# Optimization experiments

Hardware: AMD Instinct MI355X
Metric: run time of the kernel (lower is better)

Reference implementation:

```python
import jax, jax.numpy as jnp
import numpy as np

QMAX = 32767.0   # 2**15 - 1
QMIN = -32768.0  # -2**15


def setup_inputs() -> dict:
    key = jax.random.key(0)
    k_x, k_w0, k_w1, k_s, k_b = jax.random.split(key, 5)
    N, Cin, Cout = 8192, 4096, 4096
    x = jax.random.normal(k_x, (N, Cin, 1, 1), dtype=jnp.float32)
    # Fake-quantized INT8 weights: build a fp32 weight, split into dual int8 planes
    # the same way prepare_from_weight does, so w0/w1 hold integer values in [-128,127].
    W = jax.random.normal(k_w0, (Cout, Cin), dtype=jnp.float32) * 0.02
    max_abs = jnp.maximum(jnp.max(jnp.abs(W), axis=1), 1e-8)
    s0 = max_abs / 127.0
    w0 = jnp.clip(jnp.round(W / s0[:, None]), -128.0, 127.0)
    R = W - s0[:, None] * w0
    max_abs_R = jnp.max(jnp.abs(R), axis=1)
    s1 = jnp.where(max_abs_R > 1e-3, max_abs_R / 127.0, 0.0)
    w1 = jnp.where((s1 > 0)[:, None],
                   jnp.clip(jnp.round(R / jnp.where(s1 > 0, s1, 1.0)[:, None]), -128.0, 127.0),
                   0.0)
    bias = jax.random.normal(k_b, (Cout,), dtype=jnp.float32) * 0.01
    return {"x": x, "w0": w0, "w1": w1, "s0": s0, "s1": s1, "bias": bias}


def reference(x, w0, w1, s0, s1, bias):
    N, Cin, H, W_ = x.shape  # H == W_ == 1
    x2d = x.reshape(N, Cin)
    # INT16 activation fake-quant with softplus-smoothed amax
    amax = jnp.max(jnp.abs(x2d), axis=1, keepdims=True)          # [N,1]
    scale_x = jax.nn.softplus(amax) / QMAX                       # [N,1]
    xq = jnp.clip(jnp.round(x2d / scale_x), QMIN, QMAX)          # [N,Cin]
    # dual 1x1 convs == two GEMMs: [N,Cin] x [Cin,Cout]
    y0 = jnp.einsum('nc,oc->no', xq, w0)
    y1 = jnp.einsum('nc,oc->no', xq, w1)
    y = (y0 * s0[None, :] + y1 * s1[None, :]) * scale_x + bias[None, :]
    return y.reshape(N, -1, 1, 1)
```

## Files before the change

kernel.cpp:

```cpp
#include <hip/hip_runtime.h>
#include <hip/hip_fp16.h>

#define N_ROWS 8192
#define K_DIM  4096
#define M_DIM  4096
#define NT     (K_DIM / 64)
#define HT_MAX (4 * NT)

typedef __attribute__((ext_vector_type(8))) _Float16 half8;
typedef __attribute__((ext_vector_type(4))) _Float16 half4v;
typedef __attribute__((ext_vector_type(4))) float    f32x4;

__global__ __launch_bounds__(256) void prologue_kernel(
    const float* __restrict__ x,  _Float16* __restrict__ xq, float* __restrict__ sx,
    const float* __restrict__ w0, const float* __restrict__ w1,
    const float* __restrict__ s0, const float* __restrict__ s1,
    _Float16* __restrict__ wp)
{
    const int t = threadIdx.x;
    if (blockIdx.x < N_ROWS / 4) {
        const int lane = t & 63;
        const int row  = blockIdx.x * 4 + (t >> 6);
        const float4* xr4 = (const float4*)(x + (size_t)row * K_DIM);

        float4 v[16];
        float am = 0.0f;
#pragma unroll
        for (int j = 0; j < 16; ++j) {
            v[j] = xr4[j * 64 + lane];
            am = fmaxf(am, fmaxf(fmaxf(fabsf(v[j].x), fabsf(v[j].y)),
                                 fmaxf(fabsf(v[j].z), fabsf(v[j].w))));
        }
#pragma unroll
        for (int off = 32; off; off >>= 1)
            am = fmaxf(am, __shfl_xor(am, off, 64));

        const float sp    = (am > 20.0f) ? am : log1pf(expf(am));
        const float scale = sp * (1.0f / 32767.0f);
        const float inv   = 32767.0f / sp;
        if (lane == 0) sx[row] = scale;

        half4v* out4 = (half4v*)(xq + (size_t)row * K_DIM);
#pragma unroll
        for (int j = 0; j < 16; ++j) {
            half4v h;
            h[0] = (_Float16)fminf(fmaxf(rintf(v[j].x * inv), -32768.0f), 32767.0f);
            h[1] = (_Float16)fminf(fmaxf(rintf(v[j].y * inv), -32768.0f), 32767.0f);
            h[2] = (_Float16)fminf(fmaxf(rintf(v[j].z * inv), -32768.0f), 32767.0f);
            h[3] = (_Float16)fminf(fmaxf(rintf(v[j].w * inv), -32768.0f), 32767.0f);
            out4[j * 64 + lane] = h;
        }
    } else {
        const size_t gid  = (size_t)(blockIdx.x - N_ROWS / 4) * 256 + t;
        const size_t base = gid * 16;
        const int    o    = (int)(base >> 12);
        const float  a = s0[o], b = s1[o];

        const float4* p0 = (const float4*)(w0 + base);
        const float4* p1 = (const float4*)(w1 + base);
        float4 u[4], w[4];
#pragma unroll
        for (int j = 0; j < 4; ++j) { u[j] = p0[j]; w[j] = p1[j]; }

#pragma unroll
        for (int hv = 0; hv < 2; ++hv) {
            half8 h;
#pragma unroll
            for (int j = 0; j < 2; ++j) {
                const float4 uu = u[hv * 2 + j], ww = w[hv * 2 + j];
                h[j * 4 + 0] = (_Float16)(a * uu.x + b * ww.x);
                h[j * 4 + 1] = (_Float16)(a * uu.y + b * ww.y);
                h[j * 4 + 2] = (_Float16)(a * uu.z + b * ww.z);
                h[j * 4 + 3] = (_Float16)(a * uu.w + b * ww.w);
            }
            *(half8*)(wp + base + hv * 8) = h;
        }
    }
}

__device__ inline void async_load16(const void* g, void* l)
{
    __builtin_amdgcn_global_load_lds(
        (const __attribute__((address_space(1))) void*)g,
        (__attribute__((address_space(3))) void*)l, 16, 0, 0);
}

#define PHASE(BUF, QM, QN, HT, GATE)                                          \
    {                                                                         \
        half8 af[4][2], bf[2][2];                                             \
        _Pragma("unroll")                                                     \
        for (int i = 0; i < 4; ++i) {                                         \
            const int r = wm * 128 + (QM) * 64 + i * 16 + fr;                 \
            _Pragma("unroll")                                                 \
            for (int ks = 0; ks < 2; ++ks) {                                  \
                const int c = (ks * 4 + fg) ^ (r & 7);                        \
                af[i][ks] = *(const half8*)&As[BUF][r * 64 + c * 8];          \
            }                                                                 \
        }                                                                     \
        _Pragma("unroll")                                                     \
        for (int j = 0; j < 2; ++j) {                                         \
            const int r = wn * 64 + (QN) * 32 + j * 16 + fr;                  \
            _Pragma("unroll")                                                 \
            for (int ks = 0; ks < 2; ++ks) {                                  \
                const int c = (ks * 4 + fg) ^ (r & 7);                        \
                bf[j][ks] = *(const half8*)&Bs[BUF][r * 64 + c * 8];          \
            }                                                                 \
        }                                                                     \
        stage(HT);                                                            \
        __builtin_amdgcn_s_barrier();                                         \
        asm volatile("" ::: "memory");                                        \
        asm volatile("s_waitcnt lgkmcnt(0)" ::: "memory");                    \
        __builtin_amdgcn_sched_barrier(0);                                    \
        __builtin_amdgcn_s_setprio(1);                                        \
        _Pragma("unroll")                                                     \
        for (int ks = 0; ks < 2; ++ks)                                        \
            _Pragma("unroll")                                                 \
            for (int i = 0; i < 4; ++i)                                       \
                _Pragma("unroll")                                             \
                for (int j = 0; j < 2; ++j)                                   \
                    acc[(QM) * 4 + i][(QN) * 2 + j] =                         \
                        __builtin_amdgcn_mfma_f32_16x16x32_f16(               \
                            af[i][ks], bf[j][ks],                             \
                            acc[(QM) * 4 + i][(QN) * 2 + j], 0, 0, 0);        \
        __builtin_amdgcn_s_setprio(0);                                        \
        if ((GATE) == 0)                                                      \
            asm volatile("s_waitcnt vmcnt(0)" ::: "memory");                  \
        else if ((GATE) > 0)                                                  \
            asm volatile("s_waitcnt vmcnt(4)" ::: "memory");                  \
        __builtin_amdgcn_s_barrier();                                         \
        asm volatile("" ::: "memory");                                        \
    }

__global__ __launch_bounds__(512, 2) void gemm_kernel(
    const _Float16* __restrict__ A,
    const _Float16* __restrict__ B,
    const float* __restrict__ sx,
    const float* __restrict__ bias,
    float* __restrict__ out)
{
    __shared__ __align__(16) _Float16 As[2][256 * 64];
    __shared__ __align__(16) _Float16 Bs[2][256 * 64];

    const int t    = threadIdx.x;
    const int lane = t & 63;
    const int wave = t >> 6;
    const int wm   = wave >> 2;
    const int wn   = wave & 3;

    const int b2  = (blockIdx.x & 7) * 64 + (blockIdx.x >> 3);
    const int sup = b2 >> 6;
    const int loc = b2 & 63;
    const int tm  = (sup & 1) * 8 + (loc & 7);
    const int tn  = (sup >> 1) * 8 + (loc >> 3);
    const int n0  = tn * 256;
    const int o0  = tm * 256;

    const int fr = lane & 15;
    const int fg = lane >> 4;

    f32x4 acc[8][4] = {};

    auto stage = [&](int ht_) {
        if (ht_ >= HT_MAX) return;
        const int Tt  = ht_ >> 2;
        const int prt = ht_ & 3;
        const int kof = Tt * 64;
        _Float16* lbase = (prt & 1) ? &Bs[Tt & 1][0] : &As[Tt & 1][0];
        const _Float16* gbase = (prt & 1) ? B + (size_t)o0 * K_DIM
                                          : A + (size_t)n0 * K_DIM;
#pragma unroll
        for (int l = 0; l < 2; ++l) {
            const int s  = l * 512 + t;
            const int hr = s >> 3;
            const int pc = s & 7;
            int r;
            if (prt & 1) r = ((hr >> 5) << 6) | ((prt & 2) ? 32 : 0) | (hr & 31);
            else         r = ((hr >> 6) << 7) | ((prt & 2) ? 64 : 0) | (hr & 63);
            const int c = pc ^ (r & 7);
            async_load16(gbase + (size_t)r * K_DIM + kof + c * 8,
                         lbase + r * 64 + pc * 8);
        }
    };

#pragma unroll
    for (int h = 0; h < 6; ++h) stage(h);
    asm volatile("s_waitcnt vmcnt(4)" ::: "memory");
    __builtin_amdgcn_s_barrier();
    asm volatile("" ::: "memory");

    int ht = 6;
#pragma unroll 1
    for (int it = 0; it < NT / 2; ++it) {
        const int g = (it == NT / 2 - 1) ? 0 : 4;
        PHASE(0, 0, 0, ht + 0, -1)
        PHASE(0, 0, 1, ht + 1, -1)
        PHASE(0, 1, 0, ht + 2, -1)
        PHASE(0, 1, 1, ht + 3, g)
        PHASE(1, 0, 0, ht + 4, -1)
        PHASE(1, 0, 1, ht + 5, -1)
        PHASE(1, 1, 0, ht + 6, -1)
        PHASE(1, 1, 1, ht + 7, g)
        ht += 8;
    }

    float bs[4];
#pragma unroll
    for (int j = 0; j < 4; ++j)
        bs[j] = bias[o0 + wn * 64 + j * 16 + fr];
#pragma unroll
    for (int i = 0; i < 8; ++i) {
        const int nb = n0 + wm * 128 + i * 16 + fg * 4;
#pragma unroll
        for (int r = 0; r < 4; ++r) {
            const float s = sx[nb + r];
            float* orow = out + (size_t)(nb + r) * M_DIM;
#pragma unroll
            for (int j = 0; j < 4; ++j)
                orow[o0 + wn * 64 + j * 16 + fr] = acc[i][j][r] * s + bs[j];
        }
    }
}

extern "C" void kernel_launch(void* const* d_in, const int* in_sizes, int n_in,
                              void* d_out, int out_size, void* d_ws, size_t ws_size,
                              hipStream_t stream)
{
    const float* x    = (const float*)d_in[0];
    const float* w0   = (const float*)d_in[1];
    const float* w1   = (const float*)d_in[2];
    const float* s0   = (const float*)d_in[3];
    const float* s1   = (const float*)d_in[4];
    const float* bias = (const float*)d_in[5];
    float* out = (float*)d_out;

    char* ws = (char*)d_ws;
    _Float16* xq = (_Float16*)ws;
    _Float16* wp = (_Float16*)(ws + (size_t)N_ROWS * K_DIM * 2);
    float*    sx = (float*)(ws + (size_t)N_ROWS * K_DIM * 2
                               + (size_t)M_DIM * K_DIM * 2);

    prologue_kernel<<<N_ROWS / 4 + (M_DIM * K_DIM) / (256 * 16), 256, 0, stream>>>(
        x, xq, sx, w0, w1, s0, s1, wp);

    gemm_kernel<<<(N_ROWS / 256) * (M_DIM / 256), 512, 0, stream>>>(
        xq, wp, sx, bias, out);
}
```

Baseline: 605.7 us.

## Split LDS tiles by K-half and reuse B fragments across M halves

Splits the fused prologue into separate quantize and weight-fold kernels. Reorganizes the GEMM's shared-memory layout so each 64-wide K tile is stored as two 32-wide K-halves, each with its own XOR swizzle. Each phase now computes a 4x4 MFMA block over one K-half, and the B fragments loaded for the first M half are reused for the second. This cuts LDS reads per MFMA, but adds an extra kernel launch and changes the bank-conflict pattern.

```diff
diff --git a/kernel.cpp b/kernel.cpp
--- a/kernel.cpp
+++ b/kernel.cpp
@@ -11,70 +11,71 @@
 typedef __attribute__((ext_vector_type(4))) _Float16 half4v;
 typedef __attribute__((ext_vector_type(4))) float    f32x4;
 
-__global__ __launch_bounds__(256) void prologue_kernel(
-    const float* __restrict__ x,  _Float16* __restrict__ xq, float* __restrict__ sx,
+__global__ __launch_bounds__(256) void quant_kernel(
+    const float* __restrict__ x, _Float16* __restrict__ xq, float* __restrict__ sx)
+{
+    const int t    = threadIdx.x;
+    const int lane = t & 63;
+    const int row  = blockIdx.x * 4 + (t >> 6);
+    const float4* xr4 = (const float4*)(x + (size_t)row * K_DIM);
+
+    float4 v[16];
+    float am = 0.0f;
+#pragma unroll
+    for (int j = 0; j < 16; ++j) {
+        v[j] = xr4[j * 64 + lane];
+        am = fmaxf(am, fmaxf(fmaxf(fabsf(v[j].x), fabsf(v[j].y)),
+                             fmaxf(fabsf(v[j].z), fabsf(v[j].w))));
+    }
+#pragma unroll
+    for (int off = 32; off; off >>= 1)
+        am = fmaxf(am, __shfl_xor(am, off, 64));
+
+    const float sp    = (am > 20.0f) ? am : log1pf(expf(am));
+    const float scale = sp * (1.0f / 32767.0f);
+    const float inv   = 32767.0f / sp;
+    if (lane == 0) sx[row] = scale;
+
+    half4v* out4 = (half4v*)(xq + (size_t)row * K_DIM);
+#pragma unroll
+    for (int j = 0; j < 16; ++j) {
+        half4v h;
+        h[0] = (_Float16)fminf(fmaxf(rintf(v[j].x * inv), -32768.0f), 32767.0f);
+        h[1] = (_Float16)fminf(fmaxf(rintf(v[j].y * inv), -32768.0f), 32767.0f);
+        h[2] = (_Float16)fminf(fmaxf(rintf(v[j].z * inv), -32768.0f), 32767.0f);
+        h[3] = (_Float16)fminf(fmaxf(rintf(v[j].w * inv), -32768.0f), 32767.0f);
+        out4[j * 64 + lane] = h;
+    }
+}
+
+__global__ __launch_bounds__(256) void fold_kernel(
     const float* __restrict__ w0, const float* __restrict__ w1,
     const float* __restrict__ s0, const float* __restrict__ s1,
     _Float16* __restrict__ wp)
 {
-    const int t = threadIdx.x;
-    if (blockIdx.x < N_ROWS / 4) {
-        const int lane = t & 63;
-        const int row  = blockIdx.x * 4 + (t >> 6);
-        const float4* xr4 = (const float4*)(x + (size_t)row * K_DIM);
-
-        float4 v[16];
-        float am = 0.0f;
-#pragma unroll
-        for (int j = 0; j < 16; ++j) {
-            v[j] = xr4[j * 64 + lane];
-            am = fmaxf(am, fmaxf(fmaxf(fabsf(v[j].x), fabsf(v[j].y)),
-                                 fmaxf(fabsf(v[j].z), fabsf(v[j].w))));
+    const size_t gid  = (size_t)blockIdx.x * 256 + threadIdx.x;
+    const size_t base = gid * 16;
+    const int    o    = (int)(base >> 12);
+    const float  a = s0[o], b = s1[o];
+
+    const float4* p0 = (const float4*)(w0 + base);
+    const float4* p1 = (const float4*)(w1 + base);
+    float4 u[4], w[4];
+#pragma unroll
+    for (int j = 0; j < 4; ++j) { u[j] = p0[j]; w[j] = p1[j]; }
+
+#pragma unroll
+    for (int hv = 0; hv < 2; ++hv) {
+        half8 h;
+#pragma unroll
+        for (int j = 0; j < 2; ++j) {
+            const float4 uu = u[hv * 2 + j], ww = w[hv * 2 + j];
+            h[j * 4 + 0] = (_Float16)(a * uu.x + b * ww.x);
+            h[j * 4 + 1] = (_Float16)(a * uu.y + b * ww.y);
+            h[j * 4 + 2] = (_Float16)(a * uu.z + b * ww.z);
+            h[j * 4 + 3] = (_Float16)(a * uu.w + b * ww.w);
         }
-#pragma unroll
-        for (int off = 32; off; off >>= 1)
-            am = fmaxf(am, __shfl_xor(am, off, 64));
-
-        const float sp    = (am > 20.0f) ? am : log1pf(expf(am));
-        const float scale = sp * (1.0f / 32767.0f);
-        const float inv   = 32767.0f / sp;
-        if (lane == 0) sx[row] = scale;
-
-        half4v* out4 = (half4v*)(xq + (size_t)row * K_DIM);
-#pragma unroll
-        for (int j = 0; j < 16; ++j) {
-            half4v h;
-            h[0] = (_Float16)fminf(fmaxf(rintf(v[j].x * inv), -32768.0f), 32767.0f);
-            h[1] = (_Float16)fminf(fmaxf(rintf(v[j].y * inv), -32768.0f), 32767.0f);
-            h[2] = (_Float16)fminf(fmaxf(rintf(v[j].z * inv), -32768.0f), 32767.0f);
-            h[3] = (_Float16)fminf(fmaxf(rintf(v[j].w * inv), -32768.0f), 32767.0f);
-            out4[j * 64 + lane] = h;
-        }
-    } else {
-        const size_t gid  = (size_t)(blockIdx.x - N_ROWS / 4) * 256 + t;
-        const size_t base = gid * 16;
-        const int    o    = (int)(base >> 12);
-        const float  a = s0[o], b = s1[o];
-
-        const float4* p0 = (const float4*)(w0 + base);
-        const float4* p1 = (const float4*)(w1 + base);
-        float4 u[4], w[4];
-#pragma unroll
-        for (int j = 0; j < 4; ++j) { u[j] = p0[j]; w[j] = p1[j]; }
-
-#pragma unroll
-        for (int hv = 0; hv < 2; ++hv) {
-            half8 h;
-#pragma unroll
-            for (int j = 0; j < 2; ++j) {
-                const float4 uu = u[hv * 2 + j], ww = w[hv * 2 + j];
-                h[j * 4 + 0] = (_Float16)(a * uu.x + b * ww.x);
-                h[j * 4 + 1] = (_Float16)(a * uu.y + b * ww.y);
-                h[j * 4 + 2] = (_Float16)(a * uu.z + b * ww.z);
-                h[j * 4 + 3] = (_Float16)(a * uu.w + b * ww.w);
-            }
-            *(half8*)(wp + base + hv * 8) = h;
-        }
+        *(half8*)(wp + base + hv * 8) = h;
     }
 }
 
@@ -85,26 +86,21 @@
         (__attribute__((address_space(3))) void*)l, 16, 0, 0);
 }
 
-#define PHASE(BUF, QM, QN, HT, GATE)                                          \
+#define PHASE(BUF, KS, MH, RDB, HT, GATE)                                     \
     {                                                                         \
-        half8 af[4][2], bf[2][2];                                             \
-        _Pragma("unroll")                                                     \
-        for (int i = 0; i < 4; ++i) {                                         \
-            const int r = wm * 128 + (QM) * 64 + i * 16 + fr;                 \
+        if (RDB) {                                                            \
             _Pragma("unroll")                                                 \
-            for (int ks = 0; ks < 2; ++ks) {                                  \
-                const int c = (ks * 4 + fg) ^ (r & 7);                        \
-                af[i][ks] = *(const half8*)&As[BUF][r * 64 + c * 8];          \
+            for (int j = 0; j < 4; ++j) {                                     \
+                const int r = wn * 64 + j * 16 + fr;                          \
+                const int c = fg ^ ((r >> 1) & 3);                            \
+                bf[j] = *(const half8*)&Bs[BUF][(KS) * 8192 + r * 32 + c * 8];\
             }                                                                 \
         }                                                                     \
         _Pragma("unroll")                                                     \
-        for (int j = 0; j < 2; ++j) {                                         \
-            const int r = wn * 64 + (QN) * 32 + j * 16 + fr;                  \
-            _Pragma("unroll")                                                 \
-            for (int ks = 0; ks < 2; ++ks) {                                  \
-                const int c = (ks * 4 + fg) ^ (r & 7);                        \
-                bf[j][ks] = *(const half8*)&Bs[BUF][r * 64 + c * 8];          \
-            }                                                                 \
+        for (int i = 0; i < 4; ++i) {                                         \
+            const int r = wm * 128 + (MH) * 64 + i * 16 + fr;                 \
+            const int c = fg ^ ((r >> 1) & 3);                                \
+            af[i] = *(const half8*)&As[BUF][(KS) * 8192 + r * 32 + c * 8];    \
         }                                                                     \
         stage(HT);                                                            \
         __builtin_amdgcn_s_barrier();                                         \
@@ -113,15 +109,11 @@
         __builtin_amdgcn_sched_barrier(0);                                    \
         __builtin_amdgcn_s_setprio(1);                                        \
         _Pragma("unroll")                                                     \
-        for (int ks = 0; ks < 2; ++ks)                                        \
+        for (int i = 0; i < 4; ++i)                                           \
             _Pragma("unroll")                                                 \
-            for (int i = 0; i < 4; ++i)                                       \
-                _Pragma("unroll")                                             \
-                for (int j = 0; j < 2; ++j)                                   \
-                    acc[(QM) * 4 + i][(QN) * 2 + j] =                         \
-                        __builtin_amdgcn_mfma_f32_16x16x32_f16(               \
-                            af[i][ks], bf[j][ks],                             \
-                            acc[(QM) * 4 + i][(QN) * 2 + j], 0, 0, 0);        \
+            for (int j = 0; j < 4; ++j)                                       \
+                acc[(MH) * 4 + i][j] = __builtin_amdgcn_mfma_f32_16x16x32_f16(\
+                    af[i], bf[j], acc[(MH) * 4 + i][j], 0, 0, 0);             \
         __builtin_amdgcn_s_setprio(0);                                        \
         if ((GATE) == 0)                                                      \
             asm volatile("s_waitcnt vmcnt(0)" ::: "memory");                  \
@@ -138,8 +130,8 @@
     const float* __restrict__ bias,
     float* __restrict__ out)
 {
-    __shared__ __align__(16) _Float16 As[2][256 * 64];
-    __shared__ __align__(16) _Float16 Bs[2][256 * 64];
+    __shared__ __align__(16) _Float16 As[2][16384];
+    __shared__ __align__(16) _Float16 Bs[2][16384];
 
     const int t    = threadIdx.x;
     const int lane = t & 63;
@@ -164,21 +156,19 @@
         if (ht_ >= HT_MAX) return;
         const int Tt  = ht_ >> 2;
         const int prt = ht_ & 3;
-        const int kof = Tt * 64;
-        _Float16* lbase = (prt & 1) ? &Bs[Tt & 1][0] : &As[Tt & 1][0];
+        const int ks  = prt >> 1;
+        const int kof = Tt * 64 + ks * 32;
+        _Float16* lbase = ((prt & 1) ? &Bs[Tt & 1][0] : &As[Tt & 1][0]) + ks * 8192;
         const _Float16* gbase = (prt & 1) ? B + (size_t)o0 * K_DIM
                                           : A + (size_t)n0 * K_DIM;
 #pragma unroll
         for (int l = 0; l < 2; ++l) {
             const int s  = l * 512 + t;
-            const int hr = s >> 3;
-            const int pc = s & 7;
-            int r;
-            if (prt & 1) r = ((hr >> 5) << 6) | ((prt & 2) ? 32 : 0) | (hr & 31);
-            else         r = ((hr >> 6) << 7) | ((prt & 2) ? 64 : 0) | (hr & 63);
-            const int c = pc ^ (r & 7);
+            const int r  = s >> 2;
+            const int pc = s & 3;
+            const int c  = pc ^ ((r >> 1) & 3);
             async_load16(gbase + (size_t)r * K_DIM + kof + c * 8,
-                         lbase + r * 64 + pc * 8);
+                         lbase + r * 32 + pc * 8);
         }
     };
 
@@ -192,14 +182,15 @@
 #pragma unroll 1
     for (int it = 0; it < NT / 2; ++it) {
         const int g = (it == NT / 2 - 1) ? 0 : 4;
-        PHASE(0, 0, 0, ht + 0, -1)
-        PHASE(0, 0, 1, ht + 1, -1)
-        PHASE(0, 1, 0, ht + 2, -1)
-        PHASE(0, 1, 1, ht + 3, g)
-        PHASE(1, 0, 0, ht + 4, -1)
-        PHASE(1, 0, 1, ht + 5, -1)
-        PHASE(1, 1, 0, ht + 6, -1)
-        PHASE(1, 1, 1, ht + 7, g)
+        half8 af[4], bf[4];
+        PHASE(0, 0, 0, 1, ht + 0, -1)
+        PHASE(0, 0, 1, 0, ht + 1, -1)
+        PHASE(0, 1, 0, 1, ht + 2, -1)
+        PHASE(0, 1, 1, 0, ht + 3, g)
+        PHASE(1, 0, 0, 1, ht + 4, -1)
+        PHASE(1, 0, 1, 0, ht + 5, -1)
+        PHASE(1, 1, 0, 1, ht + 6, -1)
+        PHASE(1, 1, 1, 0, ht + 7, g)
         ht += 8;
     }
 
@@ -239,8 +230,8 @@
     float*    sx = (float*)(ws + (size_t)N_ROWS * K_DIM * 2
                                + (size_t)M_DIM * K_DIM * 2);
 
-    prologue_kernel<<<N_ROWS / 4 + (M_DIM * K_DIM) / (256 * 16), 256, 0, stream>>>(
-        x, xq, sx, w0, w1, s0, s1, wp);
+    quant_kernel<<<N_ROWS / 4, 256, 0, stream>>>(x, xq, sx);
+    fold_kernel<<<(M_DIM * K_DIM) / (256 * 16), 256, 0, stream>>>(w0, w1, s0, s1, wp);
 
     gemm_kernel<<<(N_ROWS / 256) * (M_DIM / 256), 512, 0, stream>>>(
         xq, wp, sx, bias, out);
```

New measurement: 569.2 us. 1.06x faster.
